# Kernel tuning notes

Measured on AMD Instinct MI355X. Metric: run time of the kernel, lower is better.

## Reference

```python
import jax, jax.numpy as jnp
import numpy as np

EPS = 1e-06


def _phi(x):
    # elu_feature_map: elu(x) + 1  (strictly positive features)
    return jax.nn.elu(x) + 1.0


def setup_inputs() -> dict:
    key = jax.random.key(0)
    k1, k2, k3 = jax.random.split(key, 3)
    N, L, H, D = 4, 4096, 12, 64
    q = jax.random.normal(k1, (N, L, H, D), dtype=jnp.float32)
    k = jax.random.normal(k2, (N, L, H, D), dtype=jnp.float32)
    v = jax.random.normal(k3, (N, L, H, D), dtype=jnp.float32)
    return {"q": q, "k": k, "v": v}


def _causal_linear_attention(q, k, v):
    qf = _phi(q)  # [N,L,H,D]
    kf = _phi(k)
    # normalizer: z_l = q_l . (sum_{s<=l} k_s) + eps
    z = jnp.einsum('nlhd,nlhd->nlh', qf, jnp.cumsum(kf, axis=1)) + EPS
    # causal_dot_product: sequential cumulative outer-product scan over L
    q_l = jnp.moveaxis(qf, 1, 0)  # [L,N,H,D]
    k_l = jnp.moveaxis(kf, 1, 0)
    v_l = jnp.moveaxis(v, 1, 0)   # [L,N,H,M]
    N, H, D = qf.shape[0], qf.shape[2], qf.shape[3]
    M = v.shape[3]
    S0 = jnp.zeros((N, H, D, M), dtype=qf.dtype)

    def step(S, qkv):
        ql, kl, vl = qkv
        S = S + jnp.einsum('nhd,nhm->nhdm', kl, vl)  # accumulate k v^T
        o = jnp.einsum('nhd,nhdm->nhm', ql, S)       # q . S
        return S, o

    _, out = jax.lax.scan(step, S0, (q_l, k_l, v_l))  # out: [L,N,H,M]
    out = jnp.moveaxis(out, 0, 1)  # [N,L,H,M]
    return out / z[..., None]


def reference(q, k, v):
    # mask=None path of LinearAttention.forward (causal linear attention)
    return _causal_linear_attention(q, k, v)
```

## Files before the change

### kernel.cpp

```cpp
#include <hip/hip_runtime.h>


#define NBATCH 4
#define LSEQ   4096
#define NHEAD  12
#define DDIM   64
#define LSTRIDE (NHEAD * DDIM)
#define NH     (NBATCH * NHEAD)
#define EPSF   1e-6f
#define CHUNK  64
#define NUMC   (LSEQ / CHUNK)
#define PPART  16
#define CPP    (NUMC / PPART)
#define SB     72

typedef __attribute__((ext_vector_type(8))) short bf16x8;
typedef __attribute__((ext_vector_type(4))) float f32x4;

__device__ __forceinline__ float phi(float x) { return x > 0.f ? x + 1.f : __expf(x); }

__device__ __forceinline__ unsigned short f2bf(float x) {
    union { float f; unsigned u; } v; v.f = x;
    unsigned r = v.u + 0x7fffu + ((v.u >> 16) & 1u);
    return (unsigned short)(r >> 16);
}
__device__ __forceinline__ float bf2f(short s) {
    union { float f; unsigned u; } v; v.u = ((unsigned)(unsigned short)s) << 16;
    return v.f;
}
__device__ __forceinline__ uint2 pack4(float4 a) {
    uint2 r;
    r.x = (unsigned)f2bf(a.x) | ((unsigned)f2bf(a.y) << 16);
    r.y = (unsigned)f2bf(a.z) | ((unsigned)f2bf(a.w) << 16);
    return r;
}

__device__ __forceinline__ float4 xpose4(float4 x, int lane) {
    const bool b0 = (lane >> 4) & 1, b1 = (lane >> 5) & 1;
    float s0 = b0 ? x.x : x.y;
    float s1 = b0 ? x.z : x.w;
    s0 = __shfl_xor(s0, 16);
    s1 = __shfl_xor(s1, 16);
    float4 y;
    if (b0) { y.x = s0;  y.y = x.y; y.z = s1;  y.w = x.w; }
    else    { y.x = x.x; y.y = s0;  y.z = x.z; y.w = s1;  }
    float t0 = b1 ? y.x : y.z;
    float t1 = b1 ? y.y : y.w;
    t0 = __shfl_xor(t0, 32);
    t1 = __shfl_xor(t1, 32);
    float4 z;
    if (b1) { z.x = t0;  z.y = t1;  z.z = y.z; z.w = y.w; }
    else    { z.x = y.x; z.y = y.y; z.z = t0;  z.w = t1;  }
    return z;
}

__global__ __launch_bounds__(256) void k_psum(const float* __restrict__ kin,
                                              const float* __restrict__ vin,
                                              float* __restrict__ kvws,
                                              float* __restrict__ ksws) {
    __shared__ short sKT[64 * SB];
    __shared__ short sVT[64 * SB];
    const int b = blockIdx.x, seq = b / PPART, p = b % PPART;
    const int n0 = seq / NHEAD, h0 = seq % NHEAD;
    const int t = threadIdx.x;
    const int lane = t & 63, w = t >> 6;
    const int nn = lane & 15, qq = lane >> 4;
    const int c4 = nn << 2;

    float4 kreg[4], vreg[4];
    auto LOADCC = [&](int cc) {
        const int gb = ((n0 * LSEQ + (p * CPP + cc) * CHUNK) * NHEAD + h0) * DDIM;
#pragma unroll
        for (int rep = 0; rep < 4; ++rep) {
            const int r16 = rep * 16 + 4 * w + qq;
            kreg[rep] = *(const float4*)(kin + gb + r16 * LSTRIDE + c4);
            vreg[rep] = *(const float4*)(vin + gb + r16 * LSTRIDE + c4);
        }
    };

    f32x4 S[4] = {{0,0,0,0},{0,0,0,0},{0,0,0,0},{0,0,0,0}};
    float ks = 0.f;
    LOADCC(0);
    for (int cc = 0; cc < CPP; ++cc) {
#pragma unroll
        for (int rep = 0; rep < 4; ++rep) {
            const int l0 = rep * 16 + 4 * w;
            float4 kk = kreg[rep];
            float4 kp = {phi(kk.x), phi(kk.y), phi(kk.z), phi(kk.w)};
            float4 kt = xpose4(kp, lane);
            *(uint2*)(sKT + (c4 + qq) * SB + l0) = pack4(kt);
            float4 vt = xpose4(vreg[rep], lane);
            *(uint2*)(sVT + (c4 + qq) * SB + l0) = pack4(vt);
        }
        __syncthreads();
        if (cc + 1 < CPP) LOADCC(cc + 1);
        const int rowM = 16 * w + nn;
        bf16x8 af0 = *(const bf16x8*)(sVT + rowM * SB + qq * 8);
        bf16x8 af1 = *(const bf16x8*)(sVT + rowM * SB + 32 + qq * 8);
#pragma unroll
        for (int ct = 0; ct < 4; ++ct) {
            bf16x8 bf0 = *(const bf16x8*)(sKT + (16 * ct + nn) * SB + qq * 8);
            bf16x8 bf1 = *(const bf16x8*)(sKT + (16 * ct + nn) * SB + 32 + qq * 8);
            S[ct] = __builtin_amdgcn_mfma_f32_16x16x32_bf16(af0, bf0, S[ct], 0, 0, 0);
            S[ct] = __builtin_amdgcn_mfma_f32_16x16x32_bf16(af1, bf1, S[ct], 0, 0, 0);
            if (ct == w) {
                float s = 0.f;
#pragma unroll
                for (int j = 0; j < 8; ++j) s += bf2f(bf0[j]) + bf2f(bf1[j]);
                s += __shfl_xor(s, 16);
                s += __shfl_xor(s, 32);
                ks += s;
            }
        }
        __syncthreads();
    }
    float* kvb = kvws + (size_t)b * (DDIM * DDIM);
#pragma unroll
    for (int ct = 0; ct < 4; ++ct)
#pragma unroll
        for (int r = 0; r < 4; ++r)
            kvb[(16 * w + 4 * qq + r) * DDIM + 16 * ct + nn] = S[ct][r];
    if (qq == 0) ksws[b * DDIM + 16 * w + nn] = ks;
}

__global__ __launch_bounds__(64) void k_scanP(float* __restrict__ kv,
                                              float* __restrict__ ksum) {
    const int bid = blockIdx.x;
    const int seq = bid >> 4, part = bid & 15;
    const int t = threadIdx.x;
    float4* base = (float4*)(kv + (size_t)seq * PPART * DDIM * DDIM) + part * 64 + t;
    float4 x[PPART];
#pragma unroll
    for (int c = 0; c < PPART; ++c) x[c] = base[c * (DDIM * DDIM / 4)];
    float4 S = {0.f, 0.f, 0.f, 0.f};
#pragma unroll
    for (int c = 0; c < PPART; ++c) {
        base[c * (DDIM * DDIM / 4)] = S;
        S.x += x[c].x; S.y += x[c].y; S.z += x[c].z; S.w += x[c].w;
    }
    if (part == 0) {
        float* kb = ksum + (size_t)seq * PPART * DDIM + t;
        float xs[PPART];
#pragma unroll
        for (int c = 0; c < PPART; ++c) xs[c] = kb[c * DDIM];
        float s = 0.f;
#pragma unroll
        for (int c = 0; c < PPART; ++c) { kb[c * DDIM] = s; s += xs[c]; }
    }
}

__global__ __launch_bounds__(256, 3) void k_fused(const float* __restrict__ qin,
                                                  const float* __restrict__ kin,
                                                  const float* __restrict__ vin,
                                                  const float* __restrict__ kvws,
                                                  const float* __restrict__ ksws,
                                                  float* __restrict__ out) {
    __shared__ short sQ [64 * SB];
    __shared__ short sKA[64 * SB];
    __shared__ short sKT[64 * SB];
    __shared__ short sVT[64 * SB];
    __shared__ short sST[64 * SB];
    __shared__ float sKs[64];
    __shared__ float sZq[64];

    const int b = blockIdx.x, seq = b / PPART, p = b % PPART;
    const int n0 = seq / NHEAD, h0 = seq % NHEAD;
    const int t = threadIdx.x;
    const int lane = t & 63, w = t >> 6;
    const int nn = lane & 15, qq = lane >> 4;
    const int c4 = nn << 2;

    if (t < 64) sKs[t] = ksws[b * DDIM + t];

    const float* Sg = kvws + (size_t)b * (DDIM * DDIM);
    f32x4 Sreg[4];
#pragma unroll
    for (int ct = 0; ct < 4; ++ct) {
#pragma unroll
        for (int r = 0; r < 4; ++r) {
            const float sv = Sg[(16 * w + 4 * qq + r) * DDIM + 16 * ct + nn];
            Sreg[ct][r] = sv;
            sST[(16 * w + 4 * qq + r) * SB + 16 * ct + nn] = (short)f2bf(sv);
        }
    }

    float4 qreg[4], kreg[4], vreg[4];
    auto LOADCC = [&](int cc) {
        const int gb = ((n0 * LSEQ + (p * CPP + cc) * CHUNK) * NHEAD + h0) * DDIM;
#pragma unroll
        for (int rep = 0; rep < 4; ++rep) {
            const int r16 = rep * 16 + 4 * w + qq;
            qreg[rep] = *(const float4*)(qin + gb + r16 * LSTRIDE + c4);
            kreg[rep] = *(const float4*)(kin + gb + r16 * LSTRIDE + c4);
            vreg[rep] = *(const float4*)(vin + gb + r16 * LSTRIDE + c4);
        }
    };
    LOADCC(0);

    for (int cc = 0; cc < CPP; ++cc) {
        const int gbase = ((n0 * LSEQ + (p * CPP + cc) * CHUNK) * NHEAD + h0) * DDIM;
#pragma unroll
        for (int rep = 0; rep < 4; ++rep) {
            const int row = rep * 16 + 4 * w + qq;
            const int l0 = rep * 16 + 4 * w;
            float4 qv = qreg[rep];
            float4 qp = {phi(qv.x), phi(qv.y), phi(qv.z), phi(qv.w)};
            *(uint2*)(sQ + row * SB + c4) = pack4(qp);
            float4 kk = kreg[rep];
            float4 kp = {phi(kk.x), phi(kk.y), phi(kk.z), phi(kk.w)};
            *(uint2*)(sKA + row * SB + c4) = pack4(kp);
            float4 kt = xpose4(kp, lane);
            *(uint2*)(sKT + (c4 + qq) * SB + l0) = pack4(kt);
            float4 vt = xpose4(vreg[rep], lane);
            *(uint2*)(sVT + (c4 + qq) * SB + l0) = pack4(vt);
        }
        __syncthreads();

        const int rowA = 16 * w + nn;
        bf16x8 qf0 = *(const bf16x8*)(sQ + rowA * SB + qq * 8);
        bf16x8 qf1 = *(const bf16x8*)(sQ + rowA * SB + 32 + qq * 8);
        float am[4][4];
        float zrow[4] = {0.f, 0.f, 0.f, 0.f};
#pragma unroll
        for (int ct = 0; ct < 4; ++ct) {
            bf16x8 kf0 = *(const bf16x8*)(sKA + (16 * ct + nn) * SB + qq * 8);
            bf16x8 kf1 = *(const bf16x8*)(sKA + (16 * ct + nn) * SB + 32 + qq * 8);
            f32x4 acc = {0.f, 0.f, 0.f, 0.f};
            acc = __builtin_amdgcn_mfma_f32_16x16x32_bf16(qf0, kf0, acc, 0, 0, 0);
            acc = __builtin_amdgcn_mfma_f32_16x16x32_bf16(qf1, kf1, acc, 0, 0, 0);
#pragma unroll
            for (int r = 0; r < 4; ++r) {
                const int ri = 16 * w + 4 * qq + r, cj = 16 * ct + nn;
                const float mval = (cj <= ri) ? acc[r] : 0.f;
                am[ct][r] = mval;
                zrow[r] += mval;
            }
        }
#pragma unroll
        for (int r = 0; r < 4; ++r) {
            float s = zrow[r];
            s += __shfl_xor(s, 1); s += __shfl_xor(s, 2);
            s += __shfl_xor(s, 4); s += __shfl_xor(s, 8);
            zrow[r] = s;
        }
        float zq = 0.f;
#pragma unroll
        for (int j = 0; j < 8; ++j) {
            zq += bf2f(qf0[j]) * sKs[qq * 8 + j];
            zq += bf2f(qf1[j]) * sKs[32 + qq * 8 + j];
        }
        zq += __shfl_xor(zq, 16);
        zq += __shfl_xor(zq, 32);

        __syncthreads();
        if (qq == 0) sZq[16 * w + nn] = zq;
#pragma unroll
        for (int ct = 0; ct < 4; ++ct)
#pragma unroll
            for (int r = 0; r < 4; ++r)
                sKA[(16 * w + 4 * qq + r) * SB + 16 * ct + nn] = (short)f2bf(am[ct][r]);
        __syncthreads();

        if (cc + 1 < CPP) LOADCC(cc + 1);

        f32x4 o[4] = {{0,0,0,0},{0,0,0,0},{0,0,0,0},{0,0,0,0}};
        bf16x8 af0 = *(const bf16x8*)(sKA + rowA * SB + qq * 8);
        bf16x8 af1 = *(const bf16x8*)(sKA + rowA * SB + 32 + qq * 8);
        bf16x8 av0 = *(const bf16x8*)(sVT + rowA * SB + qq * 8);
        bf16x8 av1 = *(const bf16x8*)(sVT + rowA * SB + 32 + qq * 8);
        float ksc = 0.f;
#pragma unroll
        for (int ct = 0; ct < 4; ++ct) {
            bf16x8 vf0 = *(const bf16x8*)(sVT + (16 * ct + nn) * SB + qq * 8);
            bf16x8 vf1 = *(const bf16x8*)(sVT + (16 * ct + nn) * SB + 32 + qq * 8);
            o[ct] = __builtin_amdgcn_mfma_f32_16x16x32_bf16(af0, vf0, o[ct], 0, 0, 0);
            o[ct] = __builtin_amdgcn_mfma_f32_16x16x32_bf16(af1, vf1, o[ct], 0, 0, 0);
            bf16x8 sf0 = *(const bf16x8*)(sST + (16 * ct + nn) * SB + qq * 8);
            bf16x8 sf1 = *(const bf16x8*)(sST + (16 * ct + nn) * SB + 32 + qq * 8);
            o[ct] = __builtin_amdgcn_mfma_f32_16x16x32_bf16(qf0, sf0, o[ct], 0, 0, 0);
            o[ct] = __builtin_amdgcn_mfma_f32_16x16x32_bf16(qf1, sf1, o[ct], 0, 0, 0);
            bf16x8 kt0 = *(const bf16x8*)(sKT + (16 * ct + nn) * SB + qq * 8);
            bf16x8 kt1 = *(const bf16x8*)(sKT + (16 * ct + nn) * SB + 32 + qq * 8);
            Sreg[ct] = __builtin_amdgcn_mfma_f32_16x16x32_bf16(av0, kt0, Sreg[ct], 0, 0, 0);
            Sreg[ct] = __builtin_amdgcn_mfma_f32_16x16x32_bf16(av1, kt1, Sreg[ct], 0, 0, 0);
            if (ct == w) {
                float s = 0.f;
#pragma unroll
                for (int j = 0; j < 8; ++j) s += bf2f(kt0[j]) + bf2f(kt1[j]);
                s += __shfl_xor(s, 16);
                s += __shfl_xor(s, 32);
                ksc = s;
            }
        }

#pragma unroll
        for (int r = 0; r < 4; ++r) {
            const int ri = 16 * w + 4 * qq + r;
            const float z = zrow[r] + sZq[ri] + EPSF;
            const float invz = 1.f / z;
#pragma unroll
            for (int ct = 0; ct < 4; ++ct)
                out[gbase + ri * LSTRIDE + 16 * ct + nn] = o[ct][r] * invz;
        }
        __syncthreads();
#pragma unroll
        for (int ct = 0; ct < 4; ++ct)
#pragma unroll
            for (int r = 0; r < 4; ++r)
                sST[(16 * w + 4 * qq + r) * SB + 16 * ct + nn] = (short)f2bf(Sreg[ct][r]);
        if (qq == 0) sKs[16 * w + nn] += ksc;
    }
}

__global__ __launch_bounds__(64) void k_seq(const float* __restrict__ qin,
                                            const float* __restrict__ kin,
                                            const float* __restrict__ vin,
                                            float* __restrict__ out) {
    const int seq = blockIdx.x;
    const int n = seq / NHEAD, h = seq % NHEAD;
    const int lane = threadIdx.x;
    float Scol[DDIM];
#pragma unroll
    for (int d = 0; d < DDIM; ++d) Scol[d] = 0.0f;
    float kc = 0.0f;
    __shared__ float qk[2 * DDIM];
    int base = (n * LSEQ * NHEAD + h) * DDIM + lane;
    for (int i = 0; i < LSEQ; ++i) {
        float qval = phi(qin[base]);
        float kval = phi(kin[base]);
        float vval = vin[base];
        kc += kval;
        float zp = qval * kc;
#pragma unroll
        for (int off = 32; off > 0; off >>= 1) zp += __shfl_xor(zp, off, 64);
        float z = zp + EPSF;
        qk[2 * lane] = kval;
        qk[2 * lane + 1] = qval;
        __syncthreads();
        const float4* qk4 = (const float4*)qk;
        float acc = 0.0f;
#pragma unroll
        for (int d2 = 0; d2 < DDIM / 2; ++d2) {
            float4 t0 = qk4[d2];
            int d = 2 * d2;
            Scol[d]     += t0.x * vval;  acc += t0.y * Scol[d];
            Scol[d + 1] += t0.z * vval;  acc += t0.w * Scol[d + 1];
        }
        out[base] = acc / z;
        base += LSTRIDE;
        __syncthreads();
    }
}

extern "C" void kernel_launch(void* const* d_in, const int* in_sizes, int n_in,
                              void* d_out, int out_size, void* d_ws, size_t ws_size,
                              hipStream_t stream) {
    const float* q = (const float*)d_in[0];
    const float* k = (const float*)d_in[1];
    const float* v = (const float*)d_in[2];
    float* out = (float*)d_out;
    float* ws  = (float*)d_ws;

    const size_t need = (size_t)NH * PPART * (DDIM * DDIM + DDIM) * sizeof(float);
    if (ws_size >= need) {
        float* kv   = ws;
        float* ksum = ws + (size_t)NH * PPART * DDIM * DDIM;
        k_psum <<<NH * PPART, 256, 0, stream>>>(k, v, kv, ksum);
        k_scanP<<<NH * PPART,  64, 0, stream>>>(kv, ksum);
        k_fused<<<NH * PPART, 256, 0, stream>>>(q, k, v, kv, ksum, out);
    } else {
        k_seq<<<NH, 64, 0, stream>>>(q, k, v, out);
    }
}
```

Measured before the change: 206.9 us.

## Fuse chunk-state pass, scan and output into one kernel with inter-block flags

Merges the partial-state kernel, the prefix-scan kernel and the fused output kernel into a single kernel. Each block publishes its local KV state and k-sum to the workspace and sets a release flag, then spin-waits on the flags of earlier partitions of the same sequence and sums their states directly. Q is also loaded straight into MFMA operand registers with phi applied, which drops the sQ shared buffer and lowers LDS use so occupancy can go to 4. This removes two kernel launches and the scan pass, but adds a flag-reset kernel and relies on all 768 blocks being co-resident, or at least scheduled in order, to avoid deadlock.

```diff
diff --git a/kernel.cpp b/kernel.cpp
--- a/kernel.cpp
+++ b/kernel.cpp
@@ -13,11 +13,16 @@
 #define PPART  16
 #define CPP    (NUMC / PPART)
 #define SB     72
+#define PAYLOAD (DDIM * DDIM + DDIM)
 
 typedef __attribute__((ext_vector_type(8))) short bf16x8;
 typedef __attribute__((ext_vector_type(4))) float f32x4;
 
 __device__ __forceinline__ float phi(float x) { return x > 0.f ? x + 1.f : __expf(x); }
+__device__ __forceinline__ float4 phi4(float4 x) {
+    float4 r = {phi(x.x), phi(x.y), phi(x.z), phi(x.w)};
+    return r;
+}
 
 __device__ __forceinline__ unsigned short f2bf(float x) {
     union { float f; unsigned u; } v; v.f = x;
@@ -33,6 +38,12 @@
     r.x = (unsigned)f2bf(a.x) | ((unsigned)f2bf(a.y) << 16);
     r.y = (unsigned)f2bf(a.z) | ((unsigned)f2bf(a.w) << 16);
     return r;
+}
+__device__ __forceinline__ bf16x8 packbf8(float4 a, float4 b) {
+    union { bf16x8 v; uint2 u[2]; } r;
+    r.u[0] = pack4(a);
+    r.u[1] = pack4(b);
+    return r.v;
 }
 
 __device__ __forceinline__ float4 xpose4(float4 x, int lane) {
@@ -54,21 +65,32 @@
     return z;
 }
 
-__global__ __launch_bounds__(256) void k_psum(const float* __restrict__ kin,
-                                              const float* __restrict__ vin,
-                                              float* __restrict__ kvws,
-                                              float* __restrict__ ksws) {
+__global__ __launch_bounds__(256) void k_init(int* __restrict__ flags) {
+    flags[blockIdx.x * 256 + threadIdx.x] = 0;
+}
+
+__global__ __launch_bounds__(256, 4) void k_la(const float* __restrict__ qin,
+                                               const float* __restrict__ kin,
+                                               const float* __restrict__ vin,
+                                               float* __restrict__ ws,
+                                               float* __restrict__ out) {
+    __shared__ short sK [64 * SB];
     __shared__ short sKT[64 * SB];
     __shared__ short sVT[64 * SB];
+    __shared__ short sST[64 * SB];
+    __shared__ float sKs[64];
+    __shared__ float sZq[64];
+
     const int b = blockIdx.x, seq = b / PPART, p = b % PPART;
     const int n0 = seq / NHEAD, h0 = seq % NHEAD;
     const int t = threadIdx.x;
     const int lane = t & 63, w = t >> 6;
     const int nn = lane & 15, qq = lane >> 4;
     const int c4 = nn << 2;
+    int* flags = (int*)(ws + (size_t)NH * PPART * PAYLOAD);
 
     float4 kreg[4], vreg[4];
-    auto LOADCC = [&](int cc) {
+    auto LOADKV = [&](int cc) {
         const int gb = ((n0 * LSEQ + (p * CPP + cc) * CHUNK) * NHEAD + h0) * DDIM;
 #pragma unroll
         for (int rep = 0; rep < 4; ++rep) {
@@ -77,23 +99,32 @@
             vreg[rep] = *(const float4*)(vin + gb + r16 * LSTRIDE + c4);
         }
     };
-
-    f32x4 S[4] = {{0,0,0,0},{0,0,0,0},{0,0,0,0},{0,0,0,0}};
-    float ks = 0.f;
-    LOADCC(0);
+    auto LOADQ = [&](int cc, bf16x8& o0, bf16x8& o1) {
+        const float* qp = qin + ((n0 * LSEQ + (p * CPP + cc) * CHUNK) * NHEAD + h0) * DDIM
+                        + (16 * w + nn) * LSTRIDE;
+        float4 a = phi4(*(const float4*)(qp + qq * 8));
+        float4 bq = phi4(*(const float4*)(qp + qq * 8 + 4));
+        float4 cq = phi4(*(const float4*)(qp + 32 + qq * 8));
+        float4 dq = phi4(*(const float4*)(qp + 32 + qq * 8 + 4));
+        o0 = packbf8(a, bq);
+        o1 = packbf8(cq, dq);
+    };
+
+    f32x4 Sown[4] = {{0,0,0,0},{0,0,0,0},{0,0,0,0},{0,0,0,0}};
+    float ksOwn = 0.f;
+    LOADKV(0);
     for (int cc = 0; cc < CPP; ++cc) {
 #pragma unroll
         for (int rep = 0; rep < 4; ++rep) {
             const int l0 = rep * 16 + 4 * w;
-            float4 kk = kreg[rep];
-            float4 kp = {phi(kk.x), phi(kk.y), phi(kk.z), phi(kk.w)};
+            float4 kp = phi4(kreg[rep]);
             float4 kt = xpose4(kp, lane);
             *(uint2*)(sKT + (c4 + qq) * SB + l0) = pack4(kt);
             float4 vt = xpose4(vreg[rep], lane);
             *(uint2*)(sVT + (c4 + qq) * SB + l0) = pack4(vt);
         }
         __syncthreads();
-        if (cc + 1 < CPP) LOADCC(cc + 1);
+        if (cc + 1 < CPP) LOADKV(cc + 1);
         const int rowM = 16 * w + nn;
         bf16x8 af0 = *(const bf16x8*)(sVT + rowM * SB + qq * 8);
         bf16x8 af1 = *(const bf16x8*)(sVT + rowM * SB + 32 + qq * 8);
@@ -101,114 +132,78 @@
         for (int ct = 0; ct < 4; ++ct) {
             bf16x8 bf0 = *(const bf16x8*)(sKT + (16 * ct + nn) * SB + qq * 8);
             bf16x8 bf1 = *(const bf16x8*)(sKT + (16 * ct + nn) * SB + 32 + qq * 8);
-            S[ct] = __builtin_amdgcn_mfma_f32_16x16x32_bf16(af0, bf0, S[ct], 0, 0, 0);
-            S[ct] = __builtin_amdgcn_mfma_f32_16x16x32_bf16(af1, bf1, S[ct], 0, 0, 0);
+            Sown[ct] = __builtin_amdgcn_mfma_f32_16x16x32_bf16(af0, bf0, Sown[ct], 0, 0, 0);
+            Sown[ct] = __builtin_amdgcn_mfma_f32_16x16x32_bf16(af1, bf1, Sown[ct], 0, 0, 0);
             if (ct == w) {
                 float s = 0.f;
 #pragma unroll
                 for (int j = 0; j < 8; ++j) s += bf2f(bf0[j]) + bf2f(bf1[j]);
                 s += __shfl_xor(s, 16);
                 s += __shfl_xor(s, 32);
-                ks += s;
+                ksOwn += s;
             }
         }
         __syncthreads();
     }
-    float* kvb = kvws + (size_t)b * (DDIM * DDIM);
+
+    float* myb = ws + (size_t)b * PAYLOAD;
 #pragma unroll
     for (int ct = 0; ct < 4; ++ct)
 #pragma unroll
         for (int r = 0; r < 4; ++r)
-            kvb[(16 * w + 4 * qq + r) * DDIM + 16 * ct + nn] = S[ct][r];
-    if (qq == 0) ksws[b * DDIM + 16 * w + nn] = ks;
-}
-
-__global__ __launch_bounds__(64) void k_scanP(float* __restrict__ kv,
-                                              float* __restrict__ ksum) {
-    const int bid = blockIdx.x;
-    const int seq = bid >> 4, part = bid & 15;
-    const int t = threadIdx.x;
-    float4* base = (float4*)(kv + (size_t)seq * PPART * DDIM * DDIM) + part * 64 + t;
-    float4 x[PPART];
-#pragma unroll
-    for (int c = 0; c < PPART; ++c) x[c] = base[c * (DDIM * DDIM / 4)];
-    float4 S = {0.f, 0.f, 0.f, 0.f};
-#pragma unroll
-    for (int c = 0; c < PPART; ++c) {
-        base[c * (DDIM * DDIM / 4)] = S;
-        S.x += x[c].x; S.y += x[c].y; S.z += x[c].z; S.w += x[c].w;
-    }
-    if (part == 0) {
-        float* kb = ksum + (size_t)seq * PPART * DDIM + t;
-        float xs[PPART];
-#pragma unroll
-        for (int c = 0; c < PPART; ++c) xs[c] = kb[c * DDIM];
-        float s = 0.f;
-#pragma unroll
-        for (int c = 0; c < PPART; ++c) { kb[c * DDIM] = s; s += xs[c]; }
-    }
-}
-
-__global__ __launch_bounds__(256, 3) void k_fused(const float* __restrict__ qin,
-                                                  const float* __restrict__ kin,
-                                                  const float* __restrict__ vin,
-                                                  const float* __restrict__ kvws,
-                                                  const float* __restrict__ ksws,
-                                                  float* __restrict__ out) {
-    __shared__ short sQ [64 * SB];
-    __shared__ short sKA[64 * SB];
-    __shared__ short sKT[64 * SB];
-    __shared__ short sVT[64 * SB];
-    __shared__ short sST[64 * SB];
-    __shared__ float sKs[64];
-    __shared__ float sZq[64];
-
-    const int b = blockIdx.x, seq = b / PPART, p = b % PPART;
-    const int n0 = seq / NHEAD, h0 = seq % NHEAD;
-    const int t = threadIdx.x;
-    const int lane = t & 63, w = t >> 6;
-    const int nn = lane & 15, qq = lane >> 4;
-    const int c4 = nn << 2;
-
-    if (t < 64) sKs[t] = ksws[b * DDIM + t];
-
-    const float* Sg = kvws + (size_t)b * (DDIM * DDIM);
-    f32x4 Sreg[4];
-#pragma unroll
-    for (int ct = 0; ct < 4; ++ct) {
-#pragma unroll
-        for (int r = 0; r < 4; ++r) {
-            const float sv = Sg[(16 * w + 4 * qq + r) * DDIM + 16 * ct + nn];
-            Sreg[ct][r] = sv;
-            sST[(16 * w + 4 * qq + r) * SB + 16 * ct + nn] = (short)f2bf(sv);
-        }
-    }
-
-    float4 qreg[4], kreg[4], vreg[4];
-    auto LOADCC = [&](int cc) {
-        const int gb = ((n0 * LSEQ + (p * CPP + cc) * CHUNK) * NHEAD + h0) * DDIM;
-#pragma unroll
-        for (int rep = 0; rep < 4; ++rep) {
-            const int r16 = rep * 16 + 4 * w + qq;
-            qreg[rep] = *(const float4*)(qin + gb + r16 * LSTRIDE + c4);
-            kreg[rep] = *(const float4*)(kin + gb + r16 * LSTRIDE + c4);
-            vreg[rep] = *(const float4*)(vin + gb + r16 * LSTRIDE + c4);
-        }
-    };
-    LOADCC(0);
-
+            __hip_atomic_store(&myb[(16 * w + 4 * qq + r) * DDIM + 16 * ct + nn],
+                               Sown[ct][r], __ATOMIC_RELAXED, __HIP_MEMORY_SCOPE_AGENT);
+    if (qq == 0)
+        __hip_atomic_store(&myb[DDIM * DDIM + 16 * w + nn], ksOwn,
+                           __ATOMIC_RELAXED, __HIP_MEMORY_SCOPE_AGENT);
+    __syncthreads();
+    if (t == 0)
+        __hip_atomic_store(&flags[b], 1, __ATOMIC_RELEASE, __HIP_MEMORY_SCOPE_AGENT);
+
+    f32x4 Sreg[4] = {{0,0,0,0},{0,0,0,0},{0,0,0,0},{0,0,0,0}};
+    float ksp = 0.f;
+    if (p > 0) {
+        if (t < p) {
+            int* fl = &flags[seq * PPART + t];
+            while (__hip_atomic_load(fl, __ATOMIC_ACQUIRE, __HIP_MEMORY_SCOPE_AGENT) == 0)
+                __builtin_amdgcn_s_sleep(8);
+        }
+        __syncthreads();
+        for (int j = 0; j < p; ++j) {
+            float* tb = ws + (size_t)(seq * PPART + j) * PAYLOAD;
+#pragma unroll
+            for (int ct = 0; ct < 4; ++ct)
+#pragma unroll
+                for (int r = 0; r < 4; ++r)
+                    Sreg[ct][r] += __hip_atomic_load(
+                        &tb[(16 * w + 4 * qq + r) * DDIM + 16 * ct + nn],
+                        __ATOMIC_RELAXED, __HIP_MEMORY_SCOPE_AGENT);
+        }
+        if (t < 64) {
+            for (int j = 0; j < p; ++j)
+                ksp += __hip_atomic_load(
+                    ws + (size_t)(seq * PPART + j) * PAYLOAD + DDIM * DDIM + t,
+                    __ATOMIC_RELAXED, __HIP_MEMORY_SCOPE_AGENT);
+        }
+    }
+    if (t < 64) sKs[t] = ksp;
+#pragma unroll
+    for (int ct = 0; ct < 4; ++ct)
+#pragma unroll
+        for (int r = 0; r < 4; ++r)
+            sST[(16 * w + 4 * qq + r) * SB + 16 * ct + nn] = (short)f2bf(Sreg[ct][r]);
+
+    bf16x8 qf0, qf1, qfn0, qfn1;
+    LOADKV(0);
+    LOADQ(0, qf0, qf1);
     for (int cc = 0; cc < CPP; ++cc) {
         const int gbase = ((n0 * LSEQ + (p * CPP + cc) * CHUNK) * NHEAD + h0) * DDIM;
 #pragma unroll
         for (int rep = 0; rep < 4; ++rep) {
             const int row = rep * 16 + 4 * w + qq;
             const int l0 = rep * 16 + 4 * w;
-            float4 qv = qreg[rep];
-            float4 qp = {phi(qv.x), phi(qv.y), phi(qv.z), phi(qv.w)};
-            *(uint2*)(sQ + row * SB + c4) = pack4(qp);
-            float4 kk = kreg[rep];
-            float4 kp = {phi(kk.x), phi(kk.y), phi(kk.z), phi(kk.w)};
-            *(uint2*)(sKA + row * SB + c4) = pack4(kp);
+            float4 kp = phi4(kreg[rep]);
+            *(uint2*)(sK + row * SB + c4) = pack4(kp);
             float4 kt = xpose4(kp, lane);
             *(uint2*)(sKT + (c4 + qq) * SB + l0) = pack4(kt);
             float4 vt = xpose4(vreg[rep], lane);
@@ -217,14 +212,12 @@
         __syncthreads();
 
         const int rowA = 16 * w + nn;
-        bf16x8 qf0 = *(const bf16x8*)(sQ + rowA * SB + qq * 8);
-        bf16x8 qf1 = *(const bf16x8*)(sQ + rowA * SB + 32 + qq * 8);
         float am[4][4];
         float zrow[4] = {0.f, 0.f, 0.f, 0.f};
 #pragma unroll
         for (int ct = 0; ct < 4; ++ct) {
-            bf16x8 kf0 = *(const bf16x8*)(sKA + (16 * ct + nn) * SB + qq * 8);
-            bf16x8 kf1 = *(const bf16x8*)(sKA + (16 * ct + nn) * SB + 32 + qq * 8);
+            bf16x8 kf0 = *(const bf16x8*)(sK + (16 * ct + nn) * SB + qq * 8);
+            bf16x8 kf1 = *(const bf16x8*)(sK + (16 * ct + nn) * SB + 32 + qq * 8);
             f32x4 acc = {0.f, 0.f, 0.f, 0.f};
             acc = __builtin_amdgcn_mfma_f32_16x16x32_bf16(qf0, kf0, acc, 0, 0, 0);
             acc = __builtin_amdgcn_mfma_f32_16x16x32_bf16(qf1, kf1, acc, 0, 0, 0);
@@ -258,14 +251,17 @@
         for (int ct = 0; ct < 4; ++ct)
 #pragma unroll
             for (int r = 0; r < 4; ++r)
-                sKA[(16 * w + 4 * qq + r) * SB + 16 * ct + nn] = (short)f2bf(am[ct][r]);
-        __syncthreads();
-
-        if (cc + 1 < CPP) LOADCC(cc + 1);
+                sK[(16 * w + 4 * qq + r) * SB + 16 * ct + nn] = (short)f2bf(am[ct][r]);
+        __syncthreads();
+
+        if (cc + 1 < CPP) {
+            LOADKV(cc + 1);
+            LOADQ(cc + 1, qfn0, qfn1);
+        }
 
         f32x4 o[4] = {{0,0,0,0},{0,0,0,0},{0,0,0,0},{0,0,0,0}};
-        bf16x8 af0 = *(const bf16x8*)(sKA + rowA * SB + qq * 8);
-        bf16x8 af1 = *(const bf16x8*)(sKA + rowA * SB + 32 + qq * 8);
+        bf16x8 af0 = *(const bf16x8*)(sK + rowA * SB + qq * 8);
+        bf16x8 af1 = *(const bf16x8*)(sK + rowA * SB + 32 + qq * 8);
         bf16x8 av0 = *(const bf16x8*)(sVT + rowA * SB + qq * 8);
         bf16x8 av1 = *(const bf16x8*)(sVT + rowA * SB + 32 + qq * 8);
         float ksc = 0.f;
@@ -309,6 +305,8 @@
             for (int r = 0; r < 4; ++r)
                 sST[(16 * w + 4 * qq + r) * SB + 16 * ct + nn] = (short)f2bf(Sreg[ct][r]);
         if (qq == 0) sKs[16 * w + nn] += ksc;
+        qf0 = qfn0;
+        qf1 = qfn1;
     }
 }
 
@@ -361,13 +359,12 @@
     float* out = (float*)d_out;
     float* ws  = (float*)d_ws;
 
-    const size_t need = (size_t)NH * PPART * (DDIM * DDIM + DDIM) * sizeof(float);
+    const size_t need = (size_t)NH * PPART * PAYLOAD * sizeof(float)
+                      + (size_t)NH * PPART * sizeof(int);
     if (ws_size >= need) {
-        float* kv   = ws;
-        float* ksum = ws + (size_t)NH * PPART * DDIM * DDIM;
-        k_psum <<<NH * PPART, 256, 0, stream>>>(k, v, kv, ksum);
-        k_scanP<<<NH * PPART,  64, 0, stream>>>(kv, ksum);
-        k_fused<<<NH * PPART, 256, 0, stream>>>(q, k, v, kv, ksum, out);
+        int* flags = (int*)(ws + (size_t)NH * PPART * PAYLOAD);
+        k_init<<<NH * PPART / 256, 256, 0, stream>>>(flags);
+        k_la<<<NH * PPART, 256, 0, stream>>>(q, k, v, ws, out);
     } else {
         k_seq<<<NH, 64, 0, stream>>>(q, k, v, out);
     }
```

New measurement: 297.5 us. 43.8% more time.

## Double sequence partitions, load Q fragments directly to registers, raise occupancy

Applied to the files above, without the earlier changes.

Doubles the number of sequence partitions so more blocks run with fewer chunks each, and adapts the prefix-scan kernel to loop over partitions in groups of eight with a fixed grid. In the fused kernel, Q is loaded straight from global memory into bf16 MFMA fragments in registers, prefetched one chunk ahead. This removes the sQ shared buffer and frees LDS for a launch bound of four blocks per CU. It also raises wave priority around the MFMA loop. The trade-offs are more partial-state workspace traffic, a longer serial scan, and uncoalesced-looking per-lane Q loads.

```diff
diff --git a/kernel.cpp b/kernel.cpp
--- a/kernel.cpp
+++ b/kernel.cpp
@@ -10,7 +10,7 @@
 #define EPSF   1e-6f
 #define CHUNK  64
 #define NUMC   (LSEQ / CHUNK)
-#define PPART  16
+#define PPART  32
 #define CPP    (NUMC / PPART)
 #define SB     72
 
@@ -18,6 +18,10 @@
 typedef __attribute__((ext_vector_type(4))) float f32x4;
 
 __device__ __forceinline__ float phi(float x) { return x > 0.f ? x + 1.f : __expf(x); }
+__device__ __forceinline__ float4 phi4(float4 x) {
+    float4 r = {phi(x.x), phi(x.y), phi(x.z), phi(x.w)};
+    return r;
+}
 
 __device__ __forceinline__ unsigned short f2bf(float x) {
     union { float f; unsigned u; } v; v.f = x;
@@ -33,6 +37,12 @@
     r.x = (unsigned)f2bf(a.x) | ((unsigned)f2bf(a.y) << 16);
     r.y = (unsigned)f2bf(a.z) | ((unsigned)f2bf(a.w) << 16);
     return r;
+}
+__device__ __forceinline__ bf16x8 packbf8(float4 a, float4 b) {
+    union { bf16x8 v; uint2 u[2]; } r;
+    r.u[0] = pack4(a);
+    r.u[1] = pack4(b);
+    return r.v;
 }
 
 __device__ __forceinline__ float4 xpose4(float4 x, int lane) {
@@ -68,7 +78,7 @@
     const int c4 = nn << 2;
 
     float4 kreg[4], vreg[4];
-    auto LOADCC = [&](int cc) {
+    auto LOADKV = [&](int cc) {
         const int gb = ((n0 * LSEQ + (p * CPP + cc) * CHUNK) * NHEAD + h0) * DDIM;
 #pragma unroll
         for (int rep = 0; rep < 4; ++rep) {
@@ -80,20 +90,19 @@
 
     f32x4 S[4] = {{0,0,0,0},{0,0,0,0},{0,0,0,0},{0,0,0,0}};
     float ks = 0.f;
-    LOADCC(0);
+    LOADKV(0);
     for (int cc = 0; cc < CPP; ++cc) {
 #pragma unroll
         for (int rep = 0; rep < 4; ++rep) {
             const int l0 = rep * 16 + 4 * w;
-            float4 kk = kreg[rep];
-            float4 kp = {phi(kk.x), phi(kk.y), phi(kk.z), phi(kk.w)};
+            float4 kp = phi4(kreg[rep]);
             float4 kt = xpose4(kp, lane);
             *(uint2*)(sKT + (c4 + qq) * SB + l0) = pack4(kt);
             float4 vt = xpose4(vreg[rep], lane);
             *(uint2*)(sVT + (c4 + qq) * SB + l0) = pack4(vt);
         }
         __syncthreads();
-        if (cc + 1 < CPP) LOADCC(cc + 1);
+        if (cc + 1 < CPP) LOADKV(cc + 1);
         const int rowM = 16 * w + nn;
         bf16x8 af0 = *(const bf16x8*)(sVT + rowM * SB + qq * 8);
         bf16x8 af1 = *(const bf16x8*)(sVT + rowM * SB + 32 + qq * 8);
@@ -126,37 +135,40 @@
 __global__ __launch_bounds__(64) void k_scanP(float* __restrict__ kv,
                                               float* __restrict__ ksum) {
     const int bid = blockIdx.x;
-    const int seq = bid >> 4, part = bid & 15;
+    const int seq = bid >> 4, part16 = bid & 15;
     const int t = threadIdx.x;
-    float4* base = (float4*)(kv + (size_t)seq * PPART * DDIM * DDIM) + part * 64 + t;
-    float4 x[PPART];
-#pragma unroll
-    for (int c = 0; c < PPART; ++c) x[c] = base[c * (DDIM * DDIM / 4)];
+    float4* base = (float4*)(kv + (size_t)seq * PPART * DDIM * DDIM) + part16 * 64 + t;
     float4 S = {0.f, 0.f, 0.f, 0.f};
-#pragma unroll
-    for (int c = 0; c < PPART; ++c) {
-        base[c * (DDIM * DDIM / 4)] = S;
-        S.x += x[c].x; S.y += x[c].y; S.z += x[c].z; S.w += x[c].w;
-    }
-    if (part == 0) {
+    for (int b0 = 0; b0 < PPART; b0 += 8) {
+        float4 x[8];
+#pragma unroll
+        for (int j = 0; j < 8; ++j) x[j] = base[(b0 + j) * (DDIM * DDIM / 4)];
+#pragma unroll
+        for (int j = 0; j < 8; ++j) {
+            base[(b0 + j) * (DDIM * DDIM / 4)] = S;
+            S.x += x[j].x; S.y += x[j].y; S.z += x[j].z; S.w += x[j].w;
+        }
+    }
+    if (part16 == 0) {
         float* kb = ksum + (size_t)seq * PPART * DDIM + t;
-        float xs[PPART];
-#pragma unroll
-        for (int c = 0; c < PPART; ++c) xs[c] = kb[c * DDIM];
         float s = 0.f;
-#pragma unroll
-        for (int c = 0; c < PPART; ++c) { kb[c * DDIM] = s; s += xs[c]; }
-    }
-}
-
-__global__ __launch_bounds__(256, 3) void k_fused(const float* __restrict__ qin,
+        for (int b0 = 0; b0 < PPART; b0 += 8) {
+            float xs[8];
+#pragma unroll
+            for (int j = 0; j < 8; ++j) xs[j] = kb[(b0 + j) * DDIM];
+#pragma unroll
+            for (int j = 0; j < 8; ++j) { kb[(b0 + j) * DDIM] = s; s += xs[j]; }
+        }
+    }
+}
+
+__global__ __launch_bounds__(256, 4) void k_fused(const float* __restrict__ qin,
                                                   const float* __restrict__ kin,
                                                   const float* __restrict__ vin,
                                                   const float* __restrict__ kvws,
                                                   const float* __restrict__ ksws,
                                                   float* __restrict__ out) {
-    __shared__ short sQ [64 * SB];
-    __shared__ short sKA[64 * SB];
+    __shared__ short sK [64 * SB];
     __shared__ short sKT[64 * SB];
     __shared__ short sVT[64 * SB];
     __shared__ short sST[64 * SB];
@@ -170,6 +182,30 @@
     const int nn = lane & 15, qq = lane >> 4;
     const int c4 = nn << 2;
 
+    float4 kreg[4], vreg[4];
+    auto LOADKV = [&](int cc) {
+        const int gb = ((n0 * LSEQ + (p * CPP + cc) * CHUNK) * NHEAD + h0) * DDIM;
+#pragma unroll
+        for (int rep = 0; rep < 4; ++rep) {
+            const int r16 = rep * 16 + 4 * w + qq;
+            kreg[rep] = *(const float4*)(kin + gb + r16 * LSTRIDE + c4);
+            vreg[rep] = *(const float4*)(vin + gb + r16 * LSTRIDE + c4);
+        }
+    };
+    auto LOADQ = [&](int cc, bf16x8& o0, bf16x8& o1) {
+        const float* qp = qin + ((n0 * LSEQ + (p * CPP + cc) * CHUNK) * NHEAD + h0) * DDIM
+                        + (16 * w + nn) * LSTRIDE;
+        float4 a = phi4(*(const float4*)(qp + qq * 8));
+        float4 bq = phi4(*(const float4*)(qp + qq * 8 + 4));
+        float4 cq = phi4(*(const float4*)(qp + 32 + qq * 8));
+        float4 dq = phi4(*(const float4*)(qp + 32 + qq * 8 + 4));
+        o0 = packbf8(a, bq);
+        o1 = packbf8(cq, dq);
+    };
+
+    bf16x8 qf0, qf1, qfn0, qfn1;
+    LOADKV(0);
+    LOADQ(0, qf0, qf1);
     if (t < 64) sKs[t] = ksws[b * DDIM + t];
 
     const float* Sg = kvws + (size_t)b * (DDIM * DDIM);
@@ -184,31 +220,14 @@
         }
     }
 
-    float4 qreg[4], kreg[4], vreg[4];
-    auto LOADCC = [&](int cc) {
-        const int gb = ((n0 * LSEQ + (p * CPP + cc) * CHUNK) * NHEAD + h0) * DDIM;
-#pragma unroll
-        for (int rep = 0; rep < 4; ++rep) {
-            const int r16 = rep * 16 + 4 * w + qq;
-            qreg[rep] = *(const float4*)(qin + gb + r16 * LSTRIDE + c4);
-            kreg[rep] = *(const float4*)(kin + gb + r16 * LSTRIDE + c4);
-            vreg[rep] = *(const float4*)(vin + gb + r16 * LSTRIDE + c4);
-        }
-    };
-    LOADCC(0);
-
     for (int cc = 0; cc < CPP; ++cc) {
         const int gbase = ((n0 * LSEQ + (p * CPP + cc) * CHUNK) * NHEAD + h0) * DDIM;
 #pragma unroll
         for (int rep = 0; rep < 4; ++rep) {
             const int row = rep * 16 + 4 * w + qq;
             const int l0 = rep * 16 + 4 * w;
-            float4 qv = qreg[rep];
-            float4 qp = {phi(qv.x), phi(qv.y), phi(qv.z), phi(qv.w)};
-            *(uint2*)(sQ + row * SB + c4) = pack4(qp);
-            float4 kk = kreg[rep];
-            float4 kp = {phi(kk.x), phi(kk.y), phi(kk.z), phi(kk.w)};
-            *(uint2*)(sKA + row * SB + c4) = pack4(kp);
+            float4 kp = phi4(kreg[rep]);
+            *(uint2*)(sK + row * SB + c4) = pack4(kp);
             float4 kt = xpose4(kp, lane);
             *(uint2*)(sKT + (c4 + qq) * SB + l0) = pack4(kt);
             float4 vt = xpose4(vreg[rep], lane);
@@ -217,14 +236,12 @@
         __syncthreads();
 
         const int rowA = 16 * w + nn;
-        bf16x8 qf0 = *(const bf16x8*)(sQ + rowA * SB + qq * 8);
-        bf16x8 qf1 = *(const bf16x8*)(sQ + rowA * SB + 32 + qq * 8);
         float am[4][4];
         float zrow[4] = {0.f, 0.f, 0.f, 0.f};
 #pragma unroll
         for (int ct = 0; ct < 4; ++ct) {
-            bf16x8 kf0 = *(const bf16x8*)(sKA + (16 * ct + nn) * SB + qq * 8);
-            bf16x8 kf1 = *(const bf16x8*)(sKA + (16 * ct + nn) * SB + 32 + qq * 8);
+            bf16x8 kf0 = *(const bf16x8*)(sK + (16 * ct + nn) * SB + qq * 8);
+            bf16x8 kf1 = *(const bf16x8*)(sK + (16 * ct + nn) * SB + 32 + qq * 8);
             f32x4 acc = {0.f, 0.f, 0.f, 0.f};
             acc = __builtin_amdgcn_mfma_f32_16x16x32_bf16(qf0, kf0, acc, 0, 0, 0);
             acc = __builtin_amdgcn_mfma_f32_16x16x32_bf16(qf1, kf1, acc, 0, 0, 0);
@@ -258,17 +275,21 @@
         for (int ct = 0; ct < 4; ++ct)
 #pragma unroll
             for (int r = 0; r < 4; ++r)
-                sKA[(16 * w + 4 * qq + r) * SB + 16 * ct + nn] = (short)f2bf(am[ct][r]);
-        __syncthreads();
-
-        if (cc + 1 < CPP) LOADCC(cc + 1);
+                sK[(16 * w + 4 * qq + r) * SB + 16 * ct + nn] = (short)f2bf(am[ct][r]);
+        __syncthreads();
+
+        if (cc + 1 < CPP) {
+            LOADKV(cc + 1);
+            LOADQ(cc + 1, qfn0, qfn1);
+        }
 
         f32x4 o[4] = {{0,0,0,0},{0,0,0,0},{0,0,0,0},{0,0,0,0}};
-        bf16x8 af0 = *(const bf16x8*)(sKA + rowA * SB + qq * 8);
-        bf16x8 af1 = *(const bf16x8*)(sKA + rowA * SB + 32 + qq * 8);
+        bf16x8 af0 = *(const bf16x8*)(sK + rowA * SB + qq * 8);
+        bf16x8 af1 = *(const bf16x8*)(sK + rowA * SB + 32 + qq * 8);
         bf16x8 av0 = *(const bf16x8*)(sVT + rowA * SB + qq * 8);
         bf16x8 av1 = *(const bf16x8*)(sVT + rowA * SB + 32 + qq * 8);
         float ksc = 0.f;
+        __builtin_amdgcn_s_setprio(1);
 #pragma unroll
         for (int ct = 0; ct < 4; ++ct) {
             bf16x8 vf0 = *(const bf16x8*)(sVT + (16 * ct + nn) * SB + qq * 8);
@@ -292,6 +313,7 @@
                 ksc = s;
             }
         }
+        __builtin_amdgcn_s_setprio(0);
 
 #pragma unroll
         for (int r = 0; r < 4; ++r) {
@@ -309,6 +331,8 @@
             for (int r = 0; r < 4; ++r)
                 sST[(16 * w + 4 * qq + r) * SB + 16 * ct + nn] = (short)f2bf(Sreg[ct][r]);
         if (qq == 0) sKs[16 * w + nn] += ksc;
+        qf0 = qfn0;
+        qf1 = qfn1;
     }
 }
 
@@ -366,7 +390,7 @@
         float* kv   = ws;
         float* ksum = ws + (size_t)NH * PPART * DDIM * DDIM;
         k_psum <<<NH * PPART, 256, 0, stream>>>(k, v, kv, ksum);
-        k_scanP<<<NH * PPART,  64, 0, stream>>>(kv, ksum);
+        k_scanP<<<NH * 16,     64, 0, stream>>>(kv, ksum);
         k_fused<<<NH * PPART, 256, 0, stream>>>(q, k, v, kv, ksum, out);
     } else {
         k_seq<<<NH, 64, 0, stream>>>(q, k, v, out);
```

Result: slower. 253.2 us (+22.4%).
